# Kernel optimization log

Hardware: AMD Instinct MI355X
Metric: run time of the kernel (lower is better)

The kernel has to match this reference:

```python
import jax, jax.numpy as jnp
import numpy as np

B = 128          # number of trees
DEPTH = 8        # complete binary tree depth -> 2^8-1 nodes per tree
NPT = 2 ** DEPTH - 1          # 255 nodes per tree
N = B * NPT                   # 32640 total nodes
E_T = NPT - 1                 # 254 edges per tree
F_IN = 64
H = 256


def _build_trees():
    """Complete binary trees; children of local node i are 2i+1, 2i+2."""
    idx = np.arange(NPT)
    depth = np.floor(np.log2(idx + 1)).astype(np.int64)
    order = (DEPTH - 1) - depth                 # leaves=0, root=DEPTH-1
    internal = idx[: NPT // 2]                  # nodes that have children
    parents = np.repeat(internal, 2)
    children = np.empty_like(parents)
    children[0::2] = 2 * internal + 1
    children[1::2] = 2 * internal + 2
    adj_local = np.stack([parents, children], axis=1)        # [E_T, 2]
    offs = (np.arange(B) * NPT)[:, None, None]
    adjacency = (adj_local[None, :, :] + offs).reshape(-1, 2)  # [B*E_T, 2]
    node_order = np.tile(order, B)                             # [N]
    edge_order = np.tile(order[parents], B)                    # [B*E_T]
    return node_order, adjacency, edge_order


def setup_inputs() -> dict:
    key = jax.random.key(0)
    ks = jax.random.split(key, 8)
    node_order, adjacency_list, edge_order = _build_trees()
    s = lambda k, shape, fan: jax.random.normal(k, shape, jnp.float32) * (fan ** -0.5)
    return {
        "features": jax.random.normal(ks[0], (N, F_IN), jnp.float32),
        "node_order": jnp.asarray(node_order, jnp.int32),
        "adjacency_list": jnp.asarray(adjacency_list, jnp.int32),
        "edge_order": jnp.asarray(edge_order, jnp.int32),
        "W_iou_w": s(ks[1], (3 * H, F_IN), F_IN),
        "W_iou_b": jnp.zeros((3 * H,), jnp.float32),
        "U_iou_w": s(ks[2], (3 * H, H), H),
        "W_f_w": s(ks[3], (H, F_IN), F_IN),
        "W_f_b": jnp.zeros((H,), jnp.float32),
        "U_f_w": s(ks[4], (H, H), H),
        "lin0_w": s(ks[5], (H, H), H),
        "lin0_b": jnp.zeros((H,), jnp.float32),
        "lin1_w": s(ks[6], (1, H), H),
        "lin1_b": jnp.zeros((1,), jnp.float32),
    }


def reference(features, node_order, adjacency_list, edge_order,
              W_iou_w, W_iou_b, U_iou_w, W_f_w, W_f_b, U_f_w,
              lin0_w, lin0_b, lin1_w, lin1_b):
    n = features.shape[0]
    parent = adjacency_list[:, 0]
    child = adjacency_list[:, 1]
    # input->gate projections, computed once for all nodes
    wx_iou = features @ W_iou_w.T + W_iou_b      # [N, 3H]
    wx_f = features @ W_f_w.T + W_f_b            # [N, H]
    h = jnp.zeros((n, H), features.dtype)
    c = jnp.zeros((n, H), features.dtype)
    # sequential bottom-up sweep over topological levels (static DEPTH levels)
    for t in range(DEPTH):
        nmask = (node_order == t)[:, None]
        emask = (edge_order == t).astype(features.dtype)[:, None]
        child_h = h[child]                       # [E, H] gather
        h_sum = jax.ops.segment_sum(child_h * emask, parent, num_segments=n)
        iou = wx_iou + h_sum @ U_iou_w.T         # [N, 3H]; h_sum==0 at level 0
        i, o, u = jnp.split(iou, 3, axis=1)
        i = jax.nn.sigmoid(i); o = jax.nn.sigmoid(o); u = jnp.tanh(u)
        f = jax.nn.sigmoid(wx_f[parent] + child_h @ U_f_w.T)  # [E, H]
        c_sum = jax.ops.segment_sum(f * c[child] * emask, parent, num_segments=n)
        new_c = i * u + c_sum
        new_h = o * jnp.tanh(new_c)
        h = jnp.where(nmask, new_h, h)
        c = jnp.where(nmask, new_c, c)
    # unbatch + mean-pool per tree (use_root=False); equal-size trees -> reshape
    x = h.reshape(B, NPT, H).mean(axis=1)        # [B, H]
    # MLP head: Linear -> ReLU -> (dropout inactive in eval) -> Linear
    x = x @ lin0_w.T + lin0_b
    x = jax.nn.relu(x)
    x = x @ lin1_w.T + lin1_b                    # [B, 1]
    return x.reshape(-1)                         # flattened, aux output is None
```

## Files before the change

kernel.cpp:

```cpp
#include <hip/hip_runtime.h>

#define B_TREES 128
#define NPT 255
#define NTOT (B_TREES * NPT)
#define FIN 64
#define HH 256

typedef short bf16x8 __attribute__((ext_vector_type(8)));
typedef float f32x4  __attribute__((ext_vector_type(4)));
typedef unsigned short u16;

__device__ __forceinline__ float sigf(float x) {
    return __frcp_rn(1.0f + __expf(-x));
}
__device__ __forceinline__ float tanh_fast(float x) {
    return __builtin_fmaf(2.0f, sigf(2.0f * x), -1.0f);
}
__device__ __forceinline__ u16 bf_hi(float v) {
    unsigned u = __float_as_uint(v);
    return (u16)((u + 0x7FFFu + ((u >> 16) & 1u)) >> 16);
}
__device__ __forceinline__ float bf_f(u16 b) { return __uint_as_float(((unsigned)b) << 16); }

__global__ __launch_bounds__(256) void pack_B(
    const float* __restrict__ Uiou, const float* __restrict__ Uf,
    const float* __restrict__ Wiou, const float* __restrict__ Wf,
    u16* __restrict__ Bhi, u16* __restrict__ Blo)
{
    int idx = blockIdx.x * 256 + threadIdx.x;
    int j    = idx & 7;
    int lane = (idx >> 3) & 63;
    int ksl  = (idx >> 9) % 10;
    int ct   = idx / 5120;
    int s = ct % 5, hb = ct / 5;
    int n = lane & 15, q = lane >> 4;
    int jH = hb * 16 + n;
    int k = (s < 4 ? ksl * 32 : 320 + ksl * 32) + q * 8 + j;

    float v = 0.0f;
    if (s == 4) {
        if (k < 576) v = Uf[(size_t)jH * HH + (k - 320)];
    } else {
        if (k < 256) {
            v = (s < 3) ? Uiou[(size_t)(s * 256 + jH) * HH + k]
                        : Uf[(size_t)jH * HH + k];
        } else {
            int kw = k - 256;
            v = (s < 3) ? Wiou[(size_t)(s * 256 + jH) * FIN + kw]
                        : 2.0f * Wf[(size_t)jH * FIN + kw];
        }
    }
    u16 hi = bf_hi(v);
    u16 lo = bf_hi(v - bf_f(hi));
    Bhi[idx] = hi;
    Blo[idx] = lo;
}

template<int NCT, bool LEAF>
__global__ __launch_bounds__(256, 2) void level_mfma(
    const float* __restrict__ feat,
    const u16* __restrict__ Bhi, const u16* __restrict__ Blo,
    const float* __restrict__ biou, const float* __restrict__ bfv,
    float* __restrict__ h, float* __restrict__ c,
    int Lt, int lg)
{
    constexpr int CSPLIT = 20 / NCT;
    constexpr int SUBS = NCT / 5;
    __shared__ char smem[73728];
    short* Ahi = (short*)smem;
    short* Alo = (short*)(smem + 36864);

    const int tid = threadIdx.x;
    const int lane = tid & 63, w = tid >> 6;
    const int cs = blockIdx.x % CSPLIT;
    const int rb = blockIdx.x / CSPLIT;
    const int m0 = rb * 32;
    const int msk = (1 << lg) - 1;
    const int ctbase = cs * 4 * NCT + w * NCT;

    const float4* Hf4 = (const float4*)h;
    const float4* Ff4 = (const float4*)feat;

    if constexpr (!LEAF) {
        for (int rep = 0; rep < 8; ++rep) {
            int flat = rep * 256 + tid;
            int m = flat >> 6, f4 = flat & 63;
            int mg = m0 + m;
            int b = mg >> lg, ii = Lt + (mg & msk);
            int gc = b * NPT + 2 * ii + 1;
            float4 h1 = Hf4[(size_t)gc * 64 + f4];
            float4 h2 = Hf4[(size_t)(gc + 1) * 64 + f4];
            float hsv[4] = {h1.x + h2.x, h1.y + h2.y, h1.z + h2.z, h1.w + h2.w};
            float hdv[4] = {h1.x - h2.x, h1.y - h2.y, h1.z - h2.z, h1.w - h2.w};
            int rt = m >> 4, lm = m & 15;
            int ks = f4 >> 3;
            int lane_ = lm + 16 * ((f4 >> 1) & 3);
            int j0 = (f4 & 1) * 4;
            ushort4 sh, sl, dh, dl;
            u16* shp = (u16*)&sh; u16* slp = (u16*)&sl;
            u16* dhp = (u16*)&dh; u16* dlp = (u16*)&dl;
#pragma unroll
            for (int e = 0; e < 4; ++e) {
                u16 a = bf_hi(hsv[e]); shp[e] = a; slp[e] = bf_hi(hsv[e] - bf_f(a));
                u16 d = bf_hi(hdv[e]); dhp[e] = d; dlp[e] = bf_hi(hdv[e] - bf_f(d));
            }
            int base_s = ((rt * 18 + ks) * 64 + lane_) * 8 + j0;
            int base_d = ((rt * 18 + ks + 10) * 64 + lane_) * 8 + j0;
            *(ushort4*)&Ahi[base_s] = sh;  *(ushort4*)&Alo[base_s] = sl;
            *(ushort4*)&Ahi[base_d] = dh;  *(ushort4*)&Alo[base_d] = dl;
        }
    }
    for (int rep = 0; rep < 2; ++rep) {
        int flat = rep * 256 + tid;
        int m = flat >> 4, f4 = flat & 15;
        int mg = m0 + m;
        int b = mg >> lg, ii = Lt + (mg & msk);
        int g = b * NPT + ii;
        float4 x4 = Ff4[(size_t)g * 16 + f4];
        float xv[4] = {x4.x, x4.y, x4.z, x4.w};
        int rt = m >> 4, lm = m & 15;
        int ks = 8 + (f4 >> 3);
        int lane_ = lm + 16 * ((f4 >> 1) & 3);
        int j0 = (f4 & 1) * 4;
        ushort4 xh, xl;
        u16* xhp = (u16*)&xh; u16* xlp = (u16*)&xl;
#pragma unroll
        for (int e = 0; e < 4; ++e) {
            u16 a = bf_hi(xv[e]); xhp[e] = a; xlp[e] = bf_hi(xv[e] - bf_f(a));
        }
        int base = ((rt * 18 + ks) * 64 + lane_) * 8 + j0;
        *(ushort4*)&Ahi[base] = xh;  *(ushort4*)&Alo[base] = xl;
    }
    __syncthreads();

    f32x4 acc[2][NCT];
#pragma unroll
    for (int rt = 0; rt < 2; ++rt)
#pragma unroll
        for (int i = 0; i < NCT; ++i) acc[rt][i] = (f32x4){0.f, 0.f, 0.f, 0.f};

    const int G0 = LEAF ? 8 : 0;
    for (int G = G0; G < 10; ++G) {
        bf16x8 ah[2], al[2];
#pragma unroll
        for (int rt = 0; rt < 2; ++rt) {
            ah[rt] = *(const bf16x8*)&Ahi[((rt * 18 + G) * 64 + lane) * 8];
            al[rt] = *(const bf16x8*)&Alo[((rt * 18 + G) * 64 + lane) * 8];
        }
#pragma unroll
        for (int ctl = 0; ctl < NCT; ++ctl) {
            if (ctl % 5 == 4) continue;
            size_t slot = (size_t)((ctbase + ctl) * 10 + G) * 512 + lane * 8;
            bf16x8 bh = *(const bf16x8*)(Bhi + slot);
            bf16x8 bl = *(const bf16x8*)(Blo + slot);
#pragma unroll
            for (int rt = 0; rt < 2; ++rt) {
                acc[rt][ctl] = __builtin_amdgcn_mfma_f32_16x16x32_bf16(ah[rt], bh, acc[rt][ctl], 0, 0, 0);
                acc[rt][ctl] = __builtin_amdgcn_mfma_f32_16x16x32_bf16(ah[rt], bl, acc[rt][ctl], 0, 0, 0);
                acc[rt][ctl] = __builtin_amdgcn_mfma_f32_16x16x32_bf16(al[rt], bh, acc[rt][ctl], 0, 0, 0);
            }
        }
    }
    if constexpr (!LEAF) {
        for (int G = 10; G < 18; ++G) {
            bf16x8 ah[2], al[2];
#pragma unroll
            for (int rt = 0; rt < 2; ++rt) {
                ah[rt] = *(const bf16x8*)&Ahi[((rt * 18 + G) * 64 + lane) * 8];
                al[rt] = *(const bf16x8*)&Alo[((rt * 18 + G) * 64 + lane) * 8];
            }
#pragma unroll
            for (int ctl = 4; ctl < NCT; ctl += 5) {
                size_t slot = (size_t)((ctbase + ctl) * 10 + (G - 10)) * 512 + lane * 8;
                bf16x8 bh = *(const bf16x8*)(Bhi + slot);
                bf16x8 bl = *(const bf16x8*)(Blo + slot);
#pragma unroll
                for (int rt = 0; rt < 2; ++rt) {
                    acc[rt][ctl] = __builtin_amdgcn_mfma_f32_16x16x32_bf16(ah[rt], bh, acc[rt][ctl], 0, 0, 0);
                    acc[rt][ctl] = __builtin_amdgcn_mfma_f32_16x16x32_bf16(ah[rt], bl, acc[rt][ctl], 0, 0, 0);
                    acc[rt][ctl] = __builtin_amdgcn_mfma_f32_16x16x32_bf16(al[rt], bh, acc[rt][ctl], 0, 0, 0);
                }
            }
        }
    }
    __syncthreads();

    float* sc = (float*)smem + w * 2592;
    const int n = lane & 15, q = lane >> 4;
#pragma unroll
    for (int sub = 0; sub < SUBS; ++sub) {
#pragma unroll
        for (int rt = 0; rt < 2; ++rt)
#pragma unroll
            for (int s = 0; s < 5; ++s) {
                f32x4 v = acc[rt][sub * 5 + s];
#pragma unroll
                for (int r = 0; r < 4; ++r)
                    sc[(rt * 16 + q * 4 + r) * 81 + s * 16 + n] = v[r];
            }
        int hb_abs = ctbase / 5 + sub;
        int jHb = hb_abs * 16;
        for (int it = 0; it < 8; ++it) {
            int idx = it * 64 + lane;
            int m = idx >> 4, jl = idx & 15;
            int jH = jHb + jl;
            float Ci  = sc[m * 81 + jl];
            float Co  = sc[m * 81 + 16 + jl];
            float Cu  = sc[m * 81 + 32 + jl];
            float Cfs = sc[m * 81 + 48 + jl];
            float Cfd = sc[m * 81 + 64 + jl];
            int mg = m0 + m;
            int b = mg >> lg, ii = Lt + (mg & msk);
            size_t g = (size_t)b * NPT + ii;
            float iv = sigf(Ci + biou[jH]);
            float ov = sigf(Co + biou[256 + jH]);
            float uv = tanh_fast(Cu + biou[512 + jH]);
            float cv;
            if constexpr (LEAF) {
                cv = iv * uv;
            } else {
                size_t gc = g + ii + 1;
                float bF = bfv[jH];
                float f1 = sigf(0.5f * (Cfs + Cfd) + bF);
                float f2 = sigf(0.5f * (Cfs - Cfd) + bF);
                cv = iv * uv + f1 * c[gc * HH + jH] + f2 * c[(gc + 1) * HH + jH];
            }
            float hv = ov * tanh_fast(cv);
            c[g * HH + jH] = cv;
            h[g * HH + jH] = hv;
        }
    }
}

__global__ __launch_bounds__(1024) void head_wide(
    const float* __restrict__ h,
    const float* __restrict__ l0w, const float* __restrict__ l0b,
    const float* __restrict__ l1w, const float* __restrict__ l1b,
    float* __restrict__ out)
{
    __shared__ float ms[4][HH];
    __shared__ float part[4][HH];
    __shared__ float red[4];
    int b = blockIdx.x, tid = threadIdx.x;
    int j = tid & 255, g = tid >> 8;
    const float* hb = h + (size_t)b * NPT * HH;

    float a = 0.f;
    for (int i = g; i < NPT; i += 4) a += hb[(size_t)i * HH + j];
    ms[g][j] = a;
    __syncthreads();
    if (g == 0) ms[0][j] = (ms[0][j] + ms[1][j] + ms[2][j] + ms[3][j]) * (1.0f / (float)NPT);
    __syncthreads();

    const float4* L0 = (const float4*)(l0w + (size_t)j * HH);
    float y = 0.f;
    for (int k4 = 16 * g; k4 < 16 * (g + 1); ++k4) {
        float4 wv = L0[k4];
        float4 m4 = ((const float4*)ms[0])[k4];
        y += wv.x * m4.x + wv.y * m4.y + wv.z * m4.z + wv.w * m4.w;
    }
    part[g][j] = y;
    __syncthreads();

    if (g == 0) {
        float yy = part[0][j] + part[1][j] + part[2][j] + part[3][j] + l0b[j];
        yy = fmaxf(yy, 0.f);
        float v = yy * l1w[j];
        for (int off = 32; off > 0; off >>= 1) v += __shfl_down(v, off, 64);
        if ((j & 63) == 0) red[j >> 6] = v;
    }
    __syncthreads();
    if (tid == 0) out[b] = red[0] + red[1] + red[2] + red[3] + l1b[0];
}

extern "C" void kernel_launch(void* const* d_in, const int* in_sizes, int n_in,
                              void* d_out, int out_size, void* d_ws, size_t ws_size,
                              hipStream_t stream)
{
    const float* feat = (const float*)d_in[0];
    const float* Wiou = (const float*)d_in[4];
    const float* biou = (const float*)d_in[5];
    const float* Uiou = (const float*)d_in[6];
    const float* Wf   = (const float*)d_in[7];
    const float* bfv  = (const float*)d_in[8];
    const float* Uf   = (const float*)d_in[9];
    const float* l0w  = (const float*)d_in[10];
    const float* l0b  = (const float*)d_in[11];
    const float* l1w  = (const float*)d_in[12];
    const float* l1b  = (const float*)d_in[13];

    float* h = (float*)d_ws;
    float* c = h + (size_t)NTOT * HH;
    u16* Bhi = (u16*)(c + (size_t)NTOT * HH);
    u16* Blo = Bhi + 409600;

    pack_B<<<1600, 256, 0, stream>>>(Uiou, Uf, Wiou, Wf, Bhi, Blo);

    level_mfma<10, true><<<1024, 256, 0, stream>>>(feat, Bhi, Blo, biou, bfv, h, c, 127, 7);
    level_mfma<10, false><<<512, 256, 0, stream>>>(feat, Bhi, Blo, biou, bfv, h, c, 63, 6);
    level_mfma<5, false><<<512, 256, 0, stream>>>(feat, Bhi, Blo, biou, bfv, h, c, 31, 5);
    level_mfma<5, false><<<256, 256, 0, stream>>>(feat, Bhi, Blo, biou, bfv, h, c, 15, 4);
    level_mfma<5, false><<<128, 256, 0, stream>>>(feat, Bhi, Blo, biou, bfv, h, c, 7, 3);
    level_mfma<5, false><<<64, 256, 0, stream>>>(feat, Bhi, Blo, biou, bfv, h, c, 3, 2);
    level_mfma<5, false><<<32, 256, 0, stream>>>(feat, Bhi, Blo, biou, bfv, h, c, 1, 1);
    level_mfma<5, false><<<16, 256, 0, stream>>>(feat, Bhi, Blo, biou, bfv, h, c, 0, 0);

    head_wide<<<B_TREES, 1024, 0, stream>>>(h, l0w, l0b, l1w, l1b, (float*)d_out);
}
```

Baseline: 280.8 us.

## Fuse upper tree levels into one kernel, FP32 leaf kernel, split head

Replaces the MFMA leaf level with a plain FP32 FMA kernel that uses a transposed W_x matrix packed alongside the bf16 weights. The five shallow levels (16 down to 1 node per tree) are fused into a single persistent kernel where each block handles two trees with block-level syncs between levels, removing four kernel launches. The pooling head is split into a 1024-block partial-sum kernel plus a small final MLP kernel to spread the h reduction over more CUs. The fused tail kernel runs only 64 blocks and leaves many CUs idle, and the leaf FP32 path trades MFMA throughput for lower setup cost.

```diff
diff --git a/kernel.cpp b/kernel.cpp
--- a/kernel.cpp
+++ b/kernel.cpp
@@ -25,38 +25,89 @@
 __global__ __launch_bounds__(256) void pack_B(
     const float* __restrict__ Uiou, const float* __restrict__ Uf,
     const float* __restrict__ Wiou, const float* __restrict__ Wf,
-    u16* __restrict__ Bhi, u16* __restrict__ Blo)
+    u16* __restrict__ Bhi, u16* __restrict__ Blo, float* __restrict__ WxT)
 {
     int idx = blockIdx.x * 256 + threadIdx.x;
-    int j    = idx & 7;
-    int lane = (idx >> 3) & 63;
-    int ksl  = (idx >> 9) % 10;
-    int ct   = idx / 5120;
-    int s = ct % 5, hb = ct / 5;
-    int n = lane & 15, q = lane >> 4;
-    int jH = hb * 16 + n;
-    int k = (s < 4 ? ksl * 32 : 320 + ksl * 32) + q * 8 + j;
-
-    float v = 0.0f;
-    if (s == 4) {
-        if (k < 576) v = Uf[(size_t)jH * HH + (k - 320)];
+    if (idx < 409600) {
+        int j    = idx & 7;
+        int lane = (idx >> 3) & 63;
+        int ksl  = (idx >> 9) % 10;
+        int ct   = idx / 5120;
+        int s = ct % 5, hb = ct / 5;
+        int n = lane & 15, q = lane >> 4;
+        int jH = hb * 16 + n;
+        int k = (s < 4 ? ksl * 32 : 320 + ksl * 32) + q * 8 + j;
+        float v = 0.0f;
+        if (s == 4) {
+            if (k < 576) v = Uf[(size_t)jH * HH + (k - 320)];
+        } else {
+            if (k < 256) {
+                v = (s < 3) ? Uiou[(size_t)(s * 256 + jH) * HH + k]
+                            : Uf[(size_t)jH * HH + k];
+            } else {
+                int kw = k - 256;
+                v = (s < 3) ? Wiou[(size_t)(s * 256 + jH) * FIN + kw]
+                            : 2.0f * Wf[(size_t)jH * FIN + kw];
+            }
+        }
+        u16 hi = bf_hi(v);
+        u16 lo = bf_hi(v - bf_f(hi));
+        Bhi[idx] = hi;
+        Blo[idx] = lo;
     } else {
-        if (k < 256) {
-            v = (s < 3) ? Uiou[(size_t)(s * 256 + jH) * HH + k]
-                        : Uf[(size_t)jH * HH + k];
-        } else {
-            int kw = k - 256;
-            v = (s < 3) ? Wiou[(size_t)(s * 256 + jH) * FIN + kw]
-                        : 2.0f * Wf[(size_t)jH * FIN + kw];
-        }
-    }
-    u16 hi = bf_hi(v);
-    u16 lo = bf_hi(v - bf_f(hi));
-    Bhi[idx] = hi;
-    Blo[idx] = lo;
-}
-
-template<int NCT, bool LEAF>
+        int idx2 = idx - 409600;
+        int k = idx2 >> 10, j = idx2 & 1023;
+        float v = (j < 768) ? Wiou[(size_t)j * 64 + k] : 2.0f * Wf[(size_t)(j - 768) * 64 + k];
+        WxT[(size_t)(k >> 2) * 4096 + j * 4 + (k & 3)] = v;
+    }
+}
+
+__global__ __launch_bounds__(256) void leaf_v2(
+    const float* __restrict__ feat,
+    const float* __restrict__ WxT, const float* __restrict__ biou,
+    float* __restrict__ h, float* __restrict__ c)
+{
+    const int NB = 16;
+    __shared__ float xs[NB][FIN];
+    int tid = threadIdx.x;
+    int l0 = blockIdx.x * NB;
+    int b = l0 >> 7;
+    int g0 = b * NPT + 127 + (l0 & 127);
+    const float* fb = feat + (size_t)g0 * FIN;
+    for (int i = tid; i < NB * FIN; i += 256) ((float*)xs)[i] = fb[i];
+    __syncthreads();
+
+    float ai[NB], ao[NB], au[NB];
+#pragma unroll
+    for (int n = 0; n < NB; ++n) { ai[n] = 0.f; ao[n] = 0.f; au[n] = 0.f; }
+
+    const float4* WxT4 = (const float4*)WxT;
+    for (int k4 = 0; k4 < 16; ++k4) {
+        size_t base = (size_t)k4 * 1024 + tid;
+        float4 wi = WxT4[base], wo = WxT4[base + 256], wu = WxT4[base + 512];
+#pragma unroll
+        for (int n = 0; n < NB; ++n) {
+            float4 x4 = ((const float4*)xs[n])[k4];
+            ai[n] += wi.x * x4.x + wi.y * x4.y + wi.z * x4.z + wi.w * x4.w;
+            ao[n] += wo.x * x4.x + wo.y * x4.y + wo.z * x4.z + wo.w * x4.w;
+            au[n] += wu.x * x4.x + wu.y * x4.y + wu.z * x4.z + wu.w * x4.w;
+        }
+    }
+
+    float bi = biou[tid], bo = biou[tid + 256], bu = biou[tid + 512];
+#pragma unroll
+    for (int n = 0; n < NB; ++n) {
+        float iv = sigf(ai[n] + bi);
+        float ov = sigf(ao[n] + bo);
+        float uv = tanh_fast(au[n] + bu);
+        float cv = iv * uv;
+        float hv = ov * tanh_fast(cv);
+        c[(size_t)(g0 + n) * HH + tid] = cv;
+        h[(size_t)(g0 + n) * HH + tid] = hv;
+    }
+}
+
+template<int NCT>
 __global__ __launch_bounds__(256, 2) void level_mfma(
     const float* __restrict__ feat,
     const u16* __restrict__ Bhi, const u16* __restrict__ Blo,
@@ -81,34 +132,32 @@
     const float4* Hf4 = (const float4*)h;
     const float4* Ff4 = (const float4*)feat;
 
-    if constexpr (!LEAF) {
-        for (int rep = 0; rep < 8; ++rep) {
-            int flat = rep * 256 + tid;
-            int m = flat >> 6, f4 = flat & 63;
-            int mg = m0 + m;
-            int b = mg >> lg, ii = Lt + (mg & msk);
-            int gc = b * NPT + 2 * ii + 1;
-            float4 h1 = Hf4[(size_t)gc * 64 + f4];
-            float4 h2 = Hf4[(size_t)(gc + 1) * 64 + f4];
-            float hsv[4] = {h1.x + h2.x, h1.y + h2.y, h1.z + h2.z, h1.w + h2.w};
-            float hdv[4] = {h1.x - h2.x, h1.y - h2.y, h1.z - h2.z, h1.w - h2.w};
-            int rt = m >> 4, lm = m & 15;
-            int ks = f4 >> 3;
-            int lane_ = lm + 16 * ((f4 >> 1) & 3);
-            int j0 = (f4 & 1) * 4;
-            ushort4 sh, sl, dh, dl;
-            u16* shp = (u16*)&sh; u16* slp = (u16*)&sl;
-            u16* dhp = (u16*)&dh; u16* dlp = (u16*)&dl;
-#pragma unroll
-            for (int e = 0; e < 4; ++e) {
-                u16 a = bf_hi(hsv[e]); shp[e] = a; slp[e] = bf_hi(hsv[e] - bf_f(a));
-                u16 d = bf_hi(hdv[e]); dhp[e] = d; dlp[e] = bf_hi(hdv[e] - bf_f(d));
-            }
-            int base_s = ((rt * 18 + ks) * 64 + lane_) * 8 + j0;
-            int base_d = ((rt * 18 + ks + 10) * 64 + lane_) * 8 + j0;
-            *(ushort4*)&Ahi[base_s] = sh;  *(ushort4*)&Alo[base_s] = sl;
-            *(ushort4*)&Ahi[base_d] = dh;  *(ushort4*)&Alo[base_d] = dl;
-        }
+    for (int rep = 0; rep < 8; ++rep) {
+        int flat = rep * 256 + tid;
+        int m = flat >> 6, f4 = flat & 63;
+        int mg = m0 + m;
+        int b = mg >> lg, ii = Lt + (mg & msk);
+        int gc = b * NPT + 2 * ii + 1;
+        float4 h1 = Hf4[(size_t)gc * 64 + f4];
+        float4 h2 = Hf4[(size_t)(gc + 1) * 64 + f4];
+        float hsv[4] = {h1.x + h2.x, h1.y + h2.y, h1.z + h2.z, h1.w + h2.w};
+        float hdv[4] = {h1.x - h2.x, h1.y - h2.y, h1.z - h2.z, h1.w - h2.w};
+        int rt = m >> 4, lm = m & 15;
+        int ks = f4 >> 3;
+        int lane_ = lm + 16 * ((f4 >> 1) & 3);
+        int j0 = (f4 & 1) * 4;
+        ushort4 sh, sl, dh, dl;
+        u16* shp = (u16*)&sh; u16* slp = (u16*)&sl;
+        u16* dhp = (u16*)&dh; u16* dlp = (u16*)&dl;
+#pragma unroll
+        for (int e = 0; e < 4; ++e) {
+            u16 a = bf_hi(hsv[e]); shp[e] = a; slp[e] = bf_hi(hsv[e] - bf_f(a));
+            u16 d = bf_hi(hdv[e]); dhp[e] = d; dlp[e] = bf_hi(hdv[e] - bf_f(d));
+        }
+        int base_s = ((rt * 18 + ks) * 64 + lane_) * 8 + j0;
+        int base_d = ((rt * 18 + ks + 10) * 64 + lane_) * 8 + j0;
+        *(ushort4*)&Ahi[base_s] = sh;  *(ushort4*)&Alo[base_s] = sl;
+        *(ushort4*)&Ahi[base_d] = dh;  *(ushort4*)&Alo[base_d] = dl;
     }
     for (int rep = 0; rep < 2; ++rep) {
         int flat = rep * 256 + tid;
@@ -139,8 +188,7 @@
 #pragma unroll
         for (int i = 0; i < NCT; ++i) acc[rt][i] = (f32x4){0.f, 0.f, 0.f, 0.f};
 
-    const int G0 = LEAF ? 8 : 0;
-    for (int G = G0; G < 10; ++G) {
+    for (int G = 0; G < 10; ++G) {
         bf16x8 ah[2], al[2];
 #pragma unroll
         for (int rt = 0; rt < 2; ++rt) {
@@ -161,25 +209,23 @@
             }
         }
     }
-    if constexpr (!LEAF) {
-        for (int G = 10; G < 18; ++G) {
-            bf16x8 ah[2], al[2];
+    for (int G = 10; G < 18; ++G) {
+        bf16x8 ah[2], al[2];
+#pragma unroll
+        for (int rt = 0; rt < 2; ++rt) {
+            ah[rt] = *(const bf16x8*)&Ahi[((rt * 18 + G) * 64 + lane) * 8];
+            al[rt] = *(const bf16x8*)&Alo[((rt * 18 + G) * 64 + lane) * 8];
+        }
+#pragma unroll
+        for (int ctl = 4; ctl < NCT; ctl += 5) {
+            size_t slot = (size_t)((ctbase + ctl) * 10 + (G - 10)) * 512 + lane * 8;
+            bf16x8 bh = *(const bf16x8*)(Bhi + slot);
+            bf16x8 bl = *(const bf16x8*)(Blo + slot);
 #pragma unroll
             for (int rt = 0; rt < 2; ++rt) {
-                ah[rt] = *(const bf16x8*)&Ahi[((rt * 18 + G) * 64 + lane) * 8];
-                al[rt] = *(const bf16x8*)&Alo[((rt * 18 + G) * 64 + lane) * 8];
-            }
-#pragma unroll
-            for (int ctl = 4; ctl < NCT; ctl += 5) {
-                size_t slot = (size_t)((ctbase + ctl) * 10 + (G - 10)) * 512 + lane * 8;
-                bf16x8 bh = *(const bf16x8*)(Bhi + slot);
-                bf16x8 bl = *(const bf16x8*)(Blo + slot);
-#pragma unroll
-                for (int rt = 0; rt < 2; ++rt) {
-                    acc[rt][ctl] = __builtin_amdgcn_mfma_f32_16x16x32_bf16(ah[rt], bh, acc[rt][ctl], 0, 0, 0);
-                    acc[rt][ctl] = __builtin_amdgcn_mfma_f32_16x16x32_bf16(ah[rt], bl, acc[rt][ctl], 0, 0, 0);
-                    acc[rt][ctl] = __builtin_amdgcn_mfma_f32_16x16x32_bf16(al[rt], bh, acc[rt][ctl], 0, 0, 0);
-                }
+                acc[rt][ctl] = __builtin_amdgcn_mfma_f32_16x16x32_bf16(ah[rt], bh, acc[rt][ctl], 0, 0, 0);
+                acc[rt][ctl] = __builtin_amdgcn_mfma_f32_16x16x32_bf16(ah[rt], bl, acc[rt][ctl], 0, 0, 0);
+                acc[rt][ctl] = __builtin_amdgcn_mfma_f32_16x16x32_bf16(al[rt], bh, acc[rt][ctl], 0, 0, 0);
             }
         }
     }
@@ -215,16 +261,11 @@
             float iv = sigf(Ci + biou[jH]);
             float ov = sigf(Co + biou[256 + jH]);
             float uv = tanh_fast(Cu + biou[512 + jH]);
-            float cv;
-            if constexpr (LEAF) {
-                cv = iv * uv;
-            } else {
-                size_t gc = g + ii + 1;
-                float bF = bfv[jH];
-                float f1 = sigf(0.5f * (Cfs + Cfd) + bF);
-                float f2 = sigf(0.5f * (Cfs - Cfd) + bF);
-                cv = iv * uv + f1 * c[gc * HH + jH] + f2 * c[(gc + 1) * HH + jH];
-            }
+            size_t gc = g + ii + 1;
+            float bF = bfv[jH];
+            float f1 = sigf(0.5f * (Cfs + Cfd) + bF);
+            float f2 = sigf(0.5f * (Cfs - Cfd) + bF);
+            float cv = iv * uv + f1 * c[gc * HH + jH] + f2 * c[(gc + 1) * HH + jH];
             float hv = ov * tanh_fast(cv);
             c[g * HH + jH] = cv;
             h[g * HH + jH] = hv;
@@ -232,43 +273,220 @@
     }
 }
 
-__global__ __launch_bounds__(1024) void head_wide(
-    const float* __restrict__ h,
+template<int NT>
+__device__ __forceinline__ void tail_level(
+    int gb0, int gb1,
+    const float* __restrict__ feat,
+    const u16* __restrict__ Bhi, const u16* __restrict__ Blo,
+    const float* __restrict__ biou, const float* __restrict__ bfv,
+    float* __restrict__ h, float* __restrict__ c, char* smem)
+{
+    short* Ahi = (short*)smem;
+    short* Alo = (short*)(smem + 36864);
+    const int tid = threadIdx.x;
+    const int lane = tid & 63, w = tid >> 6;
+    const int first = NT - 1;
+    constexpr int LOG = (NT == 16) ? 4 : (NT == 8) ? 3 : (NT == 4) ? 2 : (NT == 2) ? 1 : 0;
+
+    const float4* Hf4 = (const float4*)h;
+    const float4* Ff4 = (const float4*)feat;
+
+    for (int i = tid; i < 2 * NT * 64; i += 512) {
+        int f4 = i & 63, r = i >> 6;
+        int t = r >> LOG, lm = r & (NT - 1);
+        int gb = t ? gb1 : gb0;
+        int ii = first + lm;
+        int gc = gb + 2 * ii + 1;
+        float4 h1 = Hf4[(size_t)gc * 64 + f4];
+        float4 h2 = Hf4[(size_t)(gc + 1) * 64 + f4];
+        float hsv[4] = {h1.x + h2.x, h1.y + h2.y, h1.z + h2.z, h1.w + h2.w};
+        float hdv[4] = {h1.x - h2.x, h1.y - h2.y, h1.z - h2.z, h1.w - h2.w};
+        int ks = f4 >> 3;
+        int lane_ = lm + 16 * ((f4 >> 1) & 3);
+        int j0 = (f4 & 1) * 4;
+        ushort4 sh, sl, dh, dl;
+        u16* shp = (u16*)&sh; u16* slp = (u16*)&sl;
+        u16* dhp = (u16*)&dh; u16* dlp = (u16*)&dl;
+#pragma unroll
+        for (int e = 0; e < 4; ++e) {
+            u16 a = bf_hi(hsv[e]); shp[e] = a; slp[e] = bf_hi(hsv[e] - bf_f(a));
+            u16 d = bf_hi(hdv[e]); dhp[e] = d; dlp[e] = bf_hi(hdv[e] - bf_f(d));
+        }
+        int base_s = ((t * 18 + ks) * 64 + lane_) * 8 + j0;
+        int base_d = ((t * 18 + ks + 10) * 64 + lane_) * 8 + j0;
+        *(ushort4*)&Ahi[base_s] = sh;  *(ushort4*)&Alo[base_s] = sl;
+        *(ushort4*)&Ahi[base_d] = dh;  *(ushort4*)&Alo[base_d] = dl;
+    }
+    for (int i = tid; i < 2 * NT * 16; i += 512) {
+        int f4 = i & 15, r = i >> 4;
+        int t = r >> LOG, lm = r & (NT - 1);
+        int gb = t ? gb1 : gb0;
+        int g = gb + first + lm;
+        float4 x4 = Ff4[(size_t)g * 16 + f4];
+        float xv[4] = {x4.x, x4.y, x4.z, x4.w};
+        int ks = 8 + (f4 >> 3);
+        int lane_ = lm + 16 * ((f4 >> 1) & 3);
+        int j0 = (f4 & 1) * 4;
+        ushort4 xh, xl;
+        u16* xhp = (u16*)&xh; u16* xlp = (u16*)&xl;
+#pragma unroll
+        for (int e = 0; e < 4; ++e) {
+            u16 a = bf_hi(xv[e]); xhp[e] = a; xlp[e] = bf_hi(xv[e] - bf_f(a));
+        }
+        int base = ((t * 18 + ks) * 64 + lane_) * 8 + j0;
+        *(ushort4*)&Ahi[base] = xh;  *(ushort4*)&Alo[base] = xl;
+    }
+    __syncthreads();
+
+    float* sc = (float*)(smem + 73728) + w * 1296;
+    const int n = lane & 15, q = lane >> 4;
+
+    for (int hbi = 0; hbi < 2; ++hbi) {
+        int hb = (w & 7) + 8 * hbi;
+        f32x4 acc[2][5];
+#pragma unroll
+        for (int rt = 0; rt < 2; ++rt)
+#pragma unroll
+            for (int s = 0; s < 5; ++s) acc[rt][s] = (f32x4){0.f, 0.f, 0.f, 0.f};
+
+        for (int G = 0; G < 10; ++G) {
+            bf16x8 ah[2], al[2];
+#pragma unroll
+            for (int rt = 0; rt < 2; ++rt) {
+                ah[rt] = *(const bf16x8*)&Ahi[((rt * 18 + G) * 64 + lane) * 8];
+                al[rt] = *(const bf16x8*)&Alo[((rt * 18 + G) * 64 + lane) * 8];
+            }
+#pragma unroll
+            for (int s = 0; s < 4; ++s) {
+                size_t slot = (size_t)((hb * 5 + s) * 10 + G) * 512 + lane * 8;
+                bf16x8 bh = *(const bf16x8*)(Bhi + slot);
+                bf16x8 bl = *(const bf16x8*)(Blo + slot);
+#pragma unroll
+                for (int rt = 0; rt < 2; ++rt) {
+                    acc[rt][s] = __builtin_amdgcn_mfma_f32_16x16x32_bf16(ah[rt], bh, acc[rt][s], 0, 0, 0);
+                    acc[rt][s] = __builtin_amdgcn_mfma_f32_16x16x32_bf16(ah[rt], bl, acc[rt][s], 0, 0, 0);
+                    acc[rt][s] = __builtin_amdgcn_mfma_f32_16x16x32_bf16(al[rt], bh, acc[rt][s], 0, 0, 0);
+                }
+            }
+        }
+        for (int G = 10; G < 18; ++G) {
+            bf16x8 ah[2], al[2];
+#pragma unroll
+            for (int rt = 0; rt < 2; ++rt) {
+                ah[rt] = *(const bf16x8*)&Ahi[((rt * 18 + G) * 64 + lane) * 8];
+                al[rt] = *(const bf16x8*)&Alo[((rt * 18 + G) * 64 + lane) * 8];
+            }
+            size_t slot = (size_t)((hb * 5 + 4) * 10 + (G - 10)) * 512 + lane * 8;
+            bf16x8 bh = *(const bf16x8*)(Bhi + slot);
+            bf16x8 bl = *(const bf16x8*)(Blo + slot);
+#pragma unroll
+            for (int rt = 0; rt < 2; ++rt) {
+                acc[rt][4] = __builtin_amdgcn_mfma_f32_16x16x32_bf16(ah[rt], bh, acc[rt][4], 0, 0, 0);
+                acc[rt][4] = __builtin_amdgcn_mfma_f32_16x16x32_bf16(ah[rt], bl, acc[rt][4], 0, 0, 0);
+                acc[rt][4] = __builtin_amdgcn_mfma_f32_16x16x32_bf16(al[rt], bh, acc[rt][4], 0, 0, 0);
+            }
+        }
+
+        for (int rt = 0; rt < 2; ++rt) {
+#pragma unroll
+            for (int s = 0; s < 5; ++s) {
+                f32x4 v = acc[rt][s];
+#pragma unroll
+                for (int r = 0; r < 4; ++r)
+                    sc[(q * 4 + r) * 81 + s * 16 + n] = v[r];
+            }
+            int gb = rt ? gb1 : gb0;
+            for (int it = 0; it < 4; ++it) {
+                int idx = it * 64 + lane;
+                int lm = idx >> 4, jl = idx & 15;
+                if (lm < NT) {
+                    int jH = hb * 16 + jl;
+                    float Ci  = sc[lm * 81 + jl];
+                    float Co  = sc[lm * 81 + 16 + jl];
+                    float Cu  = sc[lm * 81 + 32 + jl];
+                    float Cfs = sc[lm * 81 + 48 + jl];
+                    float Cfd = sc[lm * 81 + 64 + jl];
+                    int ii = first + lm;
+                    size_t g = (size_t)gb + ii;
+                    size_t gc = (size_t)gb + 2 * ii + 1;
+                    float iv = sigf(Ci + biou[jH]);
+                    float ov = sigf(Co + biou[256 + jH]);
+                    float uv = tanh_fast(Cu + biou[512 + jH]);
+                    float bF = bfv[jH];
+                    float f1 = sigf(0.5f * (Cfs + Cfd) + bF);
+                    float f2 = sigf(0.5f * (Cfs - Cfd) + bF);
+                    float cv = iv * uv + f1 * c[gc * HH + jH] + f2 * c[(gc + 1) * HH + jH];
+                    float hv = ov * tanh_fast(cv);
+                    c[g * HH + jH] = cv;
+                    h[g * HH + jH] = hv;
+                }
+            }
+        }
+    }
+    __syncthreads();
+}
+
+__global__ __launch_bounds__(512, 2) void mfma_tail(
+    const float* __restrict__ feat,
+    const u16* __restrict__ Bhi, const u16* __restrict__ Blo,
+    const float* __restrict__ biou, const float* __restrict__ bfv,
+    float* __restrict__ h, float* __restrict__ c)
+{
+    __shared__ char smem[73728 + 41472];
+    int gb0 = 2 * blockIdx.x * NPT, gb1 = gb0 + NPT;
+    tail_level<16>(gb0, gb1, feat, Bhi, Blo, biou, bfv, h, c, smem);
+    tail_level<8>(gb0, gb1, feat, Bhi, Blo, biou, bfv, h, c, smem);
+    tail_level<4>(gb0, gb1, feat, Bhi, Blo, biou, bfv, h, c, smem);
+    tail_level<2>(gb0, gb1, feat, Bhi, Blo, biou, bfv, h, c, smem);
+    tail_level<1>(gb0, gb1, feat, Bhi, Blo, biou, bfv, h, c, smem);
+}
+
+__global__ __launch_bounds__(256) void head_partial(
+    const float* __restrict__ h, float* __restrict__ hp)
+{
+    int blk = blockIdx.x;
+    int b = blk >> 3, p = blk & 7, tid = threadIdx.x;
+    const float* hb = h + ((size_t)b * NPT + p * 32) * HH;
+    int rows = (p == 7) ? 31 : 32;
+    float a0 = 0.f, a1 = 0.f, a2 = 0.f, a3 = 0.f;
+    int i = 0;
+    for (; i + 3 < rows; i += 4) {
+        a0 += hb[(size_t)(i + 0) * HH + tid];
+        a1 += hb[(size_t)(i + 1) * HH + tid];
+        a2 += hb[(size_t)(i + 2) * HH + tid];
+        a3 += hb[(size_t)(i + 3) * HH + tid];
+    }
+    for (; i < rows; ++i) a0 += hb[(size_t)i * HH + tid];
+    hp[(size_t)blk * HH + tid] = a0 + a1 + a2 + a3;
+}
+
+__global__ __launch_bounds__(256) void head_final(
+    const float* __restrict__ hp,
     const float* __restrict__ l0w, const float* __restrict__ l0b,
     const float* __restrict__ l1w, const float* __restrict__ l1b,
     float* __restrict__ out)
 {
-    __shared__ float ms[4][HH];
-    __shared__ float part[4][HH];
+    __shared__ float ms[HH];
     __shared__ float red[4];
     int b = blockIdx.x, tid = threadIdx.x;
-    int j = tid & 255, g = tid >> 8;
-    const float* hb = h + (size_t)b * NPT * HH;
-
     float a = 0.f;
-    for (int i = g; i < NPT; i += 4) a += hb[(size_t)i * HH + j];
-    ms[g][j] = a;
-    __syncthreads();
-    if (g == 0) ms[0][j] = (ms[0][j] + ms[1][j] + ms[2][j] + ms[3][j]) * (1.0f / (float)NPT);
-    __syncthreads();
-
-    const float4* L0 = (const float4*)(l0w + (size_t)j * HH);
+#pragma unroll
+    for (int p = 0; p < 8; ++p) a += hp[(size_t)(b * 8 + p) * HH + tid];
+    ms[tid] = a * (1.0f / (float)NPT);
+    __syncthreads();
+
+    const float4* L0 = (const float4*)(l0w + (size_t)tid * HH);
     float y = 0.f;
-    for (int k4 = 16 * g; k4 < 16 * (g + 1); ++k4) {
+    for (int k4 = 0; k4 < 64; ++k4) {
         float4 wv = L0[k4];
-        float4 m4 = ((const float4*)ms[0])[k4];
+        float4 m4 = ((const float4*)ms)[k4];
         y += wv.x * m4.x + wv.y * m4.y + wv.z * m4.z + wv.w * m4.w;
     }
-    part[g][j] = y;
-    __syncthreads();
-
-    if (g == 0) {
-        float yy = part[0][j] + part[1][j] + part[2][j] + part[3][j] + l0b[j];
-        yy = fmaxf(yy, 0.f);
-        float v = yy * l1w[j];
-        for (int off = 32; off > 0; off >>= 1) v += __shfl_down(v, off, 64);
-        if ((j & 63) == 0) red[j >> 6] = v;
-    }
+    y += l0b[tid];
+    y = fmaxf(y, 0.f);
+    float v = y * l1w[tid];
+    for (int off = 32; off > 0; off >>= 1) v += __shfl_down(v, off, 64);
+    if ((tid & 63) == 0) red[tid >> 6] = v;
     __syncthreads();
     if (tid == 0) out[b] = red[0] + red[1] + red[2] + red[3] + l1b[0];
 }
@@ -289,21 +507,20 @@
     const float* l1w  = (const float*)d_in[12];
     const float* l1b  = (const float*)d_in[13];
 
-    float* h = (float*)d_ws;
-    float* c = h + (size_t)NTOT * HH;
-    u16* Bhi = (u16*)(c + (size_t)NTOT * HH);
-    u16* Blo = Bhi + 409600;
-
-    pack_B<<<1600, 256, 0, stream>>>(Uiou, Uf, Wiou, Wf, Bhi, Blo);
-
-    level_mfma<10, true><<<1024, 256, 0, stream>>>(feat, Bhi, Blo, biou, bfv, h, c, 127, 7);
-    level_mfma<10, false><<<512, 256, 0, stream>>>(feat, Bhi, Blo, biou, bfv, h, c, 63, 6);
-    level_mfma<5, false><<<512, 256, 0, stream>>>(feat, Bhi, Blo, biou, bfv, h, c, 31, 5);
-    level_mfma<5, false><<<256, 256, 0, stream>>>(feat, Bhi, Blo, biou, bfv, h, c, 15, 4);
-    level_mfma<5, false><<<128, 256, 0, stream>>>(feat, Bhi, Blo, biou, bfv, h, c, 7, 3);
-    level_mfma<5, false><<<64, 256, 0, stream>>>(feat, Bhi, Blo, biou, bfv, h, c, 3, 2);
-    level_mfma<5, false><<<32, 256, 0, stream>>>(feat, Bhi, Blo, biou, bfv, h, c, 1, 1);
-    level_mfma<5, false><<<16, 256, 0, stream>>>(feat, Bhi, Blo, biou, bfv, h, c, 0, 0);
-
-    head_wide<<<B_TREES, 1024, 0, stream>>>(h, l0w, l0b, l1w, l1b, (float*)d_out);
-}
+    float* h  = (float*)d_ws;
+    float* c  = h + (size_t)NTOT * HH;
+    u16* Bhi  = (u16*)(c + (size_t)NTOT * HH);
+    u16* Blo  = Bhi + 409600;
+    float* WxT = (float*)(Blo + 409600);
+    float* hp  = WxT + 65536;
+
+    pack_B<<<1856, 256, 0, stream>>>(Uiou, Uf, Wiou, Wf, Bhi, Blo, WxT);
+
+    leaf_v2<<<1024, 256, 0, stream>>>(feat, WxT, biou, h, c);
+    level_mfma<10><<<512, 256, 0, stream>>>(feat, Bhi, Blo, biou, bfv, h, c, 63, 6);
+    level_mfma<5><<<512, 256, 0, stream>>>(feat, Bhi, Blo, biou, bfv, h, c, 31, 5);
+    mfma_tail<<<64, 512, 0, stream>>>(feat, Bhi, Blo, biou, bfv, h, c);
+
+    head_partial<<<1024, 256, 0, stream>>>(h, hp);
+    head_final<<<B_TREES, 256, 0, stream>>>(hp, l0w, l0b, l1w, l1b, (float*)d_out);
+}
```

New measurement: 340.2 us. 1.21x slower.
